# Performance work log

Hardware: AMD Instinct MI355X
Metric: run time of the kernel (lower is better)

Reference implementation:

```python
import jax, jax.numpy as jnp
import numpy as np

HEAD_DIM = 64
CLIP = 64  # clipping_distance
B, S = 32, 1024


def setup_inputs() -> dict:
    key = jax.random.key(0)
    kq, kk, kv, km, kt = jax.random.split(key, 5)
    q = jax.random.normal(kq, (B, S, HEAD_DIM), dtype=jnp.float32)
    k = jax.random.normal(kk, (B, S, HEAD_DIM), dtype=jnp.float32)
    v = jax.random.normal(kv, (B, S, HEAD_DIM), dtype=jnp.float32)
    mask = jax.random.randint(km, (B, S, S), 0, 2).astype(jnp.bool_)
    pos_table = jax.random.normal(kt, (2 * CLIP + 1, HEAD_DIM), dtype=jnp.float32)
    return {"q": q, "k": k, "v": v, "mask": mask, "pos_table": pos_table}


def reference(q, k, v, mask, pos_table):
    scaling = 1.0 / np.sqrt(HEAD_DIM).astype(np.float32)
    Sq, Sk = q.shape[1], k.shape[1]
    # relative positions k_idx - q_idx, clipped to [-CLIP, CLIP]
    rel = jnp.arange(Sk)[None, :] - jnp.arange(Sq)[:, None]      # [Sq, Sk]
    idx = jnp.clip(rel, -CLIP, CLIP) + CLIP                      # [Sq, Sk]
    pe = pos_table[idx]                                          # [Sq, Sk, D]
    # content logits + relative positional logits
    logits = jnp.einsum('bqd,bkd->bqk', q, k) + jnp.einsum('bqd,qkd->bqk', q, pe)
    logits = logits * scaling
    logits = jnp.where(mask, -jnp.inf, logits)
    attn = jax.nn.softmax(logits, axis=-1)                       # [B, Sq, Sk]
    return jnp.einsum('bqk,bkd->bqd', attn, v)
```

## Files before the change

kernel.cpp:

```cpp
#include <hip/hip_runtime.h>
#include <stdint.h>

#define BATCH 32
#define SEQ   1024
#define DIM   64
#define NKT   (SEQ / 64)

typedef uint16_t u16;
typedef uint32_t u32;
typedef unsigned long long u64;
typedef __attribute__((ext_vector_type(8))) __bf16 bf16x8;
typedef __attribute__((ext_vector_type(4))) float  f32x4;
typedef __attribute__((ext_vector_type(4))) u32    u32x4;

__device__ __forceinline__ float fexp2(float x) {
#if __has_builtin(__builtin_amdgcn_exp2f)
    return __builtin_amdgcn_exp2f(x);
#else
    return exp2f(x);
#endif
}

__device__ __forceinline__ u16 f2bf(float f) {
    u32 x = __builtin_bit_cast(u32, f);
    x += 0x7FFFu + ((x >> 16) & 1u);
    return (u16)(x >> 16);
}

__device__ __forceinline__ bf16x8 cvt8(const float* __restrict__ p) {
    f32x4 a = *reinterpret_cast<const f32x4*>(p);
    f32x4 b = *reinterpret_cast<const f32x4*>(p + 4);
    u16 t[8];
    t[0] = f2bf(a[0]); t[1] = f2bf(a[1]); t[2] = f2bf(a[2]); t[3] = f2bf(a[3]);
    t[4] = f2bf(b[0]); t[5] = f2bf(b[1]); t[6] = f2bf(b[2]); t[7] = f2bf(b[3]);
    return __builtin_bit_cast(bf16x8, *reinterpret_cast<u32x4*>(t));
}

__device__ __forceinline__ bf16x8 cvt8s(const float* __restrict__ p, float s) {
    f32x4 a = *reinterpret_cast<const f32x4*>(p);
    f32x4 b = *reinterpret_cast<const f32x4*>(p + 4);
    u16 t[8];
    t[0] = f2bf(a[0] * s); t[1] = f2bf(a[1] * s); t[2] = f2bf(a[2] * s); t[3] = f2bf(a[3] * s);
    t[4] = f2bf(b[0] * s); t[5] = f2bf(b[1] * s); t[6] = f2bf(b[2] * s); t[7] = f2bf(b[3] * s);
    return __builtin_bit_cast(bf16x8, *reinterpret_cast<u32x4*>(t));
}

__device__ __forceinline__ bf16x8 ldg8(const u16* p) {
    u32x4 u = *reinterpret_cast<const u32x4*>(p);
    return __builtin_bit_cast(bf16x8, u);
}

__global__ __launch_bounds__(256) void prep_kernel(
    const float* __restrict__ kg, const float* __restrict__ vg,
    const int* __restrict__ mask, u16* __restrict__ kb,
    u16* __restrict__ vtb_, u64* __restrict__ bits) {
    __shared__ u16 tile[64][72];
    const int t    = threadIdx.x;
    const int wave = t >> 6;
    const int lane = t & 63;
    const int wid  = blockIdx.x * 4 + wave;

    u32x4 cur = *reinterpret_cast<const u32x4*>(
        mask + (size_t)(wid >> 2) * SEQ + (wid & 3) * 256 + lane * 4);
#pragma unroll 1
    for (int it = 0; it < 4; ++it) {
        const int rg = wid + it * 32768;
        u32x4 nxt;
        if (it < 3) {
            const int rg2 = wid + (it + 1) * 32768;
            nxt = *reinterpret_cast<const u32x4*>(
                mask + (size_t)(rg2 >> 2) * SEQ + (rg2 & 3) * 256 + lane * 4);
        }
        int nib = (cur[0] != 0) | ((cur[1] != 0) << 1) |
                  ((cur[2] != 0) << 2) | ((cur[3] != 0) << 3);
        u64 b0 = __ballot(nib & 1);
        u64 b1 = __ballot(nib & 2);
        u64 b2 = __ballot(nib & 4);
        u64 b3 = __ballot(nib & 8);
        if (lane < 4) {
            u64 w = (lane == 0) ? b0 : (lane == 1) ? b1 : (lane == 2) ? b2 : b3;
            bits[(size_t)rg * 4 + lane] = w;
        }
        cur = nxt;
    }

    if (blockIdx.x < 512) {
        const int b  = blockIdx.x >> 4;
        const int k0 = (blockIdx.x & 15) * 64;

        {
            int kk = t >> 2;
            int d0 = (t & 3) * 16;
            const float* src = kg + ((size_t)b * SEQ + k0 + kk) * DIM + d0;
            u16 tmp[16];
#pragma unroll
            for (int i = 0; i < 4; ++i) {
                f32x4 a = *reinterpret_cast<const f32x4*>(src + i * 4);
                tmp[i * 4 + 0] = f2bf(a[0]); tmp[i * 4 + 1] = f2bf(a[1]);
                tmp[i * 4 + 2] = f2bf(a[2]); tmp[i * 4 + 3] = f2bf(a[3]);
            }
            u16* dst = kb + ((size_t)b * SEQ + k0 + kk) * DIM + d0;
            *reinterpret_cast<u32x4*>(dst)     = *reinterpret_cast<u32x4*>(tmp);
            *reinterpret_cast<u32x4*>(dst + 8) = *reinterpret_cast<u32x4*>(tmp + 8);
        }

        const float* vb  = vg  + (size_t)b * SEQ * DIM;
        u16*         vtb = vtb_ + (size_t)b * DIM * SEQ;
        {
            int kk = t >> 2;
            int d0 = (t & 3) * 16;
            const float* src = vb + (size_t)(k0 + kk) * DIM + d0;
            u16 tmp[16];
#pragma unroll
            for (int i = 0; i < 4; ++i) {
                f32x4 a = *reinterpret_cast<const f32x4*>(src + i * 4);
                tmp[i * 4 + 0] = f2bf(a[0]); tmp[i * 4 + 1] = f2bf(a[1]);
                tmp[i * 4 + 2] = f2bf(a[2]); tmp[i * 4 + 3] = f2bf(a[3]);
            }
            *reinterpret_cast<u32x4*>(&tile[kk][d0])     = *reinterpret_cast<u32x4*>(tmp);
            *reinterpret_cast<u32x4*>(&tile[kk][d0 + 8]) = *reinterpret_cast<u32x4*>(tmp + 8);
        }
        __syncthreads();
#pragma unroll
        for (int i = 0; i < 2; ++i) {
            int d  = t / 8 + i * 32;
            int ks = (t % 8) * 8;
            u16 tmp[8];
#pragma unroll
            for (int j = 0; j < 8; ++j) tmp[j] = tile[ks + j][d];
            *reinterpret_cast<u32x4*>(vtb + (size_t)d * SEQ + k0 + ks) =
                *reinterpret_cast<u32x4*>(tmp);
        }
    }
}

__global__ __launch_bounds__(512, 4) void attn_fast2(
    const float* __restrict__ qg, const u16* __restrict__ kbf,
    const u16* __restrict__ vt, const u64* __restrict__ mbits,
    const float* __restrict__ ptg, float* __restrict__ outg) {
    __shared__ float qp[64][132];
    __shared__ u16   plds[8][16][72];

    const int b    = blockIdx.y;
    const int q0   = blockIdx.x * 64;
    const int tid  = threadIdx.x;
    const int wave = tid >> 6;
    const int lane = tid & 63;
    const int wq   = wave & 3;
    const int wk   = wave >> 2;
    const int quad = lane >> 4;
    const int c16  = lane & 15;

    const float SC = 0.125f * 1.44269504088896340736f;

    const float* qb = qg + ((size_t)b * SEQ + q0) * DIM;

    const bf16x8 qA0 = cvt8s(qb + (size_t)(wq * 16 + c16) * DIM + quad * 8, SC);
    const bf16x8 qA1 = cvt8s(qb + (size_t)(wq * 16 + c16) * DIM + 32 + quad * 8, SC);

    const size_t rowbase = (size_t)b * SEQ + q0 + wq * 16 + quad * 4;
    u64 w2[2][4];
#pragma unroll
    for (int gg = 0; gg < 2; ++gg)
#pragma unroll
        for (int r = 0; r < 4; ++r)
            w2[gg][r] = mbits[((rowbase + r) * 4 + (wk * 2 + gg)) * 4 + (c16 & 3)];

    {
        const int jt0 = wk ? 5 : 0, jt1 = wk ? 9 : 5;
        for (int jt = jt0; jt < jt1; ++jt) {
            int j0 = jt * 16;
            int jr = min(j0 + c16, 128);
            bf16x8 b0 = cvt8(ptg + (size_t)jr * DIM + quad * 8);
            bf16x8 b1 = cvt8(ptg + (size_t)jr * DIM + 32 + quad * 8);
            f32x4 acc = {0.f, 0.f, 0.f, 0.f};
            acc = __builtin_amdgcn_mfma_f32_16x16x32_bf16(qA0, b0, acc, 0, 0, 0);
            acc = __builtin_amdgcn_mfma_f32_16x16x32_bf16(qA1, b1, acc, 0, 0, 0);
            int jcol = j0 + c16;
            if (jcol <= 128) {
#pragma unroll
                for (int r = 0; r < 4; ++r)
                    qp[wq * 16 + quad * 4 + r][jcol] = acc[r];
            }
        }
    }
    __syncthreads();

    const u16* kb_base  = kbf + (size_t)b * SEQ * DIM;
    const u16* vtb_base = vt  + (size_t)b * DIM * SEQ;

    float m_run[4], l_run[4];
    f32x4 O[4];
#pragma unroll
    for (int r = 0; r < 4; ++r) { m_run[r] = -1e30f; l_run[r] = 0.f; }
#pragma unroll
    for (int d = 0; d < 4; ++d) O[d] = f32x4{0.f, 0.f, 0.f, 0.f};

#pragma unroll
    for (int gg = 0; gg < 2; ++gg) {
#pragma unroll 1
        for (int t = 0; t < 4; ++t) {
            const int kt = wk * 8 + gg * 4 + t;
            const int k0 = kt * 64;

            f32x4 S[4];
            __builtin_amdgcn_s_setprio(1);
#pragma unroll
            for (int sub = 0; sub < 4; ++sub) {
                const u16* kr = kb_base + (size_t)(k0 + sub * 16 + c16) * DIM;
                bf16x8 kf0 = ldg8(kr + quad * 8);
                bf16x8 kf1 = ldg8(kr + 32 + quad * 8);
                f32x4 acc = {0.f, 0.f, 0.f, 0.f};
                acc = __builtin_amdgcn_mfma_f32_16x16x32_bf16(qA0, kf0, acc, 0, 0, 0);
                acc = __builtin_amdgcn_mfma_f32_16x16x32_bf16(qA1, kf1, acc, 0, 0, 0);
                S[sub] = acc;
            }
            __builtin_amdgcn_s_setprio(0);

            float sv[4][4];
#pragma unroll
            for (int r = 0; r < 4; ++r) {
                const int row_l = quad * 4 + r;
                const int row_g = q0 + wq * 16 + row_l;
                const u64 wr = w2[gg][r] >> (t * 16 + (c16 >> 2));
#pragma unroll
                for (int sub = 0; sub < 4; ++sub) {
                    int col_g = k0 + sub * 16 + c16;
                    int rel = col_g - row_g;
                    rel = rel < -64 ? -64 : (rel > 64 ? 64 : rel);
                    float x = S[sub][r] + qp[wq * 16 + row_l][rel + 64];
                    u32 bit = (u32)(wr >> (sub * 4)) & 1u;
                    sv[sub][r] = bit ? -1e30f : x;
                }
            }

            float m_new[4];
            bool need = false;
#pragma unroll
            for (int r = 0; r < 4; ++r) {
                float rmax = fmaxf(fmaxf(sv[0][r], sv[1][r]), fmaxf(sv[2][r], sv[3][r]));
                rmax = fmaxf(rmax, __shfl_xor(rmax, 1));
                rmax = fmaxf(rmax, __shfl_xor(rmax, 2));
                rmax = fmaxf(rmax, __shfl_xor(rmax, 4));
                rmax = fmaxf(rmax, __shfl_xor(rmax, 8));
                m_new[r] = fmaxf(m_run[r], rmax);
                need |= (m_new[r] > m_run[r]);
            }
            if (__any(need)) {
#pragma unroll
                for (int r = 0; r < 4; ++r) {
                    float alpha = fexp2(m_run[r] - m_new[r]);
                    l_run[r] *= alpha;
#pragma unroll
                    for (int d = 0; d < 4; ++d) O[d][r] *= alpha;
                }
            }
#pragma unroll
            for (int r = 0; r < 4; ++r) {
                m_run[r] = m_new[r];
                float rs = 0.f;
#pragma unroll
                for (int sub = 0; sub < 4; ++sub) {
                    float e = fexp2(sv[sub][r] - m_new[r]);
                    rs += e;
                    plds[wave][quad * 4 + r][sub * 16 + c16] = f2bf(e);
                }
                rs += __shfl_xor(rs, 1);
                rs += __shfl_xor(rs, 2);
                rs += __shfl_xor(rs, 4);
                rs += __shfl_xor(rs, 8);
                l_run[r] += rs;
            }

            bf16x8 pA0 = *reinterpret_cast<bf16x8*>(&plds[wave][c16][quad * 8]);
            bf16x8 pA1 = *reinterpret_cast<bf16x8*>(&plds[wave][c16][32 + quad * 8]);
            __builtin_amdgcn_s_setprio(1);
#pragma unroll
            for (int d = 0; d < 4; ++d) {
                const u16* vr = vtb_base + (size_t)(d * 16 + c16) * SEQ + k0;
                bf16x8 vf0 = ldg8(vr + quad * 8);
                bf16x8 vf1 = ldg8(vr + 32 + quad * 8);
                O[d] = __builtin_amdgcn_mfma_f32_16x16x32_bf16(pA0, vf0, O[d], 0, 0, 0);
                O[d] = __builtin_amdgcn_mfma_f32_16x16x32_bf16(pA1, vf1, O[d], 0, 0, 0);
            }
            __builtin_amdgcn_s_setprio(0);
        }
    }

    __syncthreads();
    float* cmb = &qp[0][0];
    const int cbase = (wq * 64 + lane) * 24;
    if (wk == 1) {
#pragma unroll
        for (int r = 0; r < 4; ++r) {
            cmb[cbase + r]     = m_run[r];
            cmb[cbase + 4 + r] = l_run[r];
        }
#pragma unroll
        for (int d = 0; d < 4; ++d)
#pragma unroll
            for (int r = 0; r < 4; ++r)
                cmb[cbase + 8 + d * 4 + r] = O[d][r];
    }
    __syncthreads();
    if (wk == 0) {
        float* ob = outg + ((size_t)b * SEQ + q0) * DIM;
#pragma unroll
        for (int r = 0; r < 4; ++r) {
            float m1 = cmb[cbase + r];
            float l1 = cmb[cbase + 4 + r];
            float mm = fmaxf(m_run[r], m1);
            float a0 = fexp2(m_run[r] - mm);
            float a1 = fexp2(m1 - mm);
            float inv = 1.f / (l_run[r] * a0 + l1 * a1);
            int row_l = wq * 16 + quad * 4 + r;
#pragma unroll
            for (int d = 0; d < 4; ++d) {
                float o = O[d][r] * a0 + cmb[cbase + 8 + d * 4 + r] * a1;
                ob[(size_t)row_l * DIM + d * 16 + c16] = o * inv;
            }
        }
    }
}

__global__ __launch_bounds__(256) void vt_kernel(const float* __restrict__ v,
                                                 u16* __restrict__ vt) {
    __shared__ u16 tile[64][72];
    const int b  = blockIdx.y;
    const int k0 = blockIdx.x * 64;
    const int t  = threadIdx.x;
    const float* vb  = v  + (size_t)b * SEQ * DIM;
    u16*         vtb = vt + (size_t)b * DIM * SEQ;

    {
        int kk = t >> 2;
        int d0 = (t & 3) * 16;
        const float* src = vb + (size_t)(k0 + kk) * DIM + d0;
        u16 tmp[16];
#pragma unroll
        for (int i = 0; i < 4; ++i) {
            f32x4 a = *reinterpret_cast<const f32x4*>(src + i * 4);
            tmp[i * 4 + 0] = f2bf(a[0]); tmp[i * 4 + 1] = f2bf(a[1]);
            tmp[i * 4 + 2] = f2bf(a[2]); tmp[i * 4 + 3] = f2bf(a[3]);
        }
        *reinterpret_cast<u32x4*>(&tile[kk][d0])     = *reinterpret_cast<u32x4*>(tmp);
        *reinterpret_cast<u32x4*>(&tile[kk][d0 + 8]) = *reinterpret_cast<u32x4*>(tmp + 8);
    }
    __syncthreads();
#pragma unroll
    for (int i = 0; i < 2; ++i) {
        int d  = t / 8 + i * 32;
        int ks = (t % 8) * 8;
        u16 tmp[8];
#pragma unroll
        for (int j = 0; j < 8; ++j) tmp[j] = tile[ks + j][d];
        *reinterpret_cast<u32x4*>(vtb + (size_t)d * SEQ + k0 + ks) =
            *reinterpret_cast<u32x4*>(tmp);
    }
}

template <bool USE_VT>
__global__ __launch_bounds__(256, 2) void attn_kernel(
    const float* __restrict__ qg, const float* __restrict__ kg,
    const void* __restrict__ vgv, const int* __restrict__ maskg,
    const float* __restrict__ ptg, float* __restrict__ outg) {
    __shared__ float qp[64][132];
    __shared__ int   mlds[4][16][68];
    __shared__ u16   plds[4][16][72];

    const int b    = blockIdx.y;
    const int q0   = blockIdx.x * 64;
    const int tid  = threadIdx.x;
    const int wave = tid >> 6;
    const int lane = tid & 63;
    const int quad = lane >> 4;
    const int c16  = lane & 15;

    const float* qb = qg + ((size_t)b * SEQ + q0) * DIM;
    const float* kb = kg + (size_t)b * SEQ * DIM;
    const int*   mb = maskg + ((size_t)b * SEQ + q0) * SEQ;

    const bf16x8 qA0 = cvt8(qb + (size_t)(wave * 16 + c16) * DIM + quad * 8);
    const bf16x8 qA1 = cvt8(qb + (size_t)(wave * 16 + c16) * DIM + 32 + quad * 8);

    for (int jt = 0; jt < 9; ++jt) {
        int j0 = jt * 16;
        int jr = min(j0 + c16, 128);
        bf16x8 b0 = cvt8(ptg + (size_t)jr * DIM + quad * 8);
        bf16x8 b1 = cvt8(ptg + (size_t)jr * DIM + 32 + quad * 8);
        f32x4 acc = {0.f, 0.f, 0.f, 0.f};
        acc = __builtin_amdgcn_mfma_f32_16x16x32_bf16(qA0, b0, acc, 0, 0, 0);
        acc = __builtin_amdgcn_mfma_f32_16x16x32_bf16(qA1, b1, acc, 0, 0, 0);
        int jcol = j0 + c16;
        if (jcol <= 128) {
#pragma unroll
            for (int r = 0; r < 4; ++r)
                qp[wave * 16 + quad * 4 + r][jcol] = acc[r];
        }
    }

    float m_run[4], l_run[4];
    f32x4 O[4];
#pragma unroll
    for (int r = 0; r < 4; ++r) { m_run[r] = -1e30f; l_run[r] = 0.f; }
#pragma unroll
    for (int d = 0; d < 4; ++d) O[d] = f32x4{0.f, 0.f, 0.f, 0.f};

#pragma unroll 1
    for (int kt = 0; kt < NKT; ++kt) {
        const int k0 = kt * 64;
        {
            int row_l = lane >> 2;
            const int* mrow = mb + (size_t)(wave * 16 + row_l) * SEQ + k0;
#pragma unroll
            for (int i = 0; i < 4; ++i) {
                int seg = (lane & 3) + i * 4;
                *reinterpret_cast<u32x4*>(&mlds[wave][row_l][seg * 4]) =
                    *reinterpret_cast<const u32x4*>(mrow + seg * 4);
            }
        }

        f32x4 S[4];
#pragma unroll
        for (int sub = 0; sub < 4; ++sub) {
            const float* kr = kb + (size_t)(k0 + sub * 16 + c16) * DIM;
            bf16x8 kb0 = cvt8(kr + quad * 8);
            bf16x8 kb1 = cvt8(kr + 32 + quad * 8);
            f32x4 acc = {0.f, 0.f, 0.f, 0.f};
            acc = __builtin_amdgcn_mfma_f32_16x16x32_bf16(qA0, kb0, acc, 0, 0, 0);
            acc = __builtin_amdgcn_mfma_f32_16x16x32_bf16(qA1, kb1, acc, 0, 0, 0);
            S[sub] = acc;
        }

        float sv[4][4];
#pragma unroll
        for (int sub = 0; sub < 4; ++sub) {
#pragma unroll
            for (int r = 0; r < 4; ++r) {
                int row_l = quad * 4 + r;
                int row_g = q0 + wave * 16 + row_l;
                int col_g = k0 + sub * 16 + c16;
                int rel = col_g - row_g;
                rel = rel < -64 ? -64 : (rel > 64 ? 64 : rel);
                float x = (S[sub][r] + qp[wave * 16 + row_l][rel + 64]) * 0.125f;
                int mv = mlds[wave][row_l][sub * 16 + c16];
                sv[sub][r] = mv ? -1e30f : x;
            }
        }

        float m_new[4], alpha[4];
#pragma unroll
        for (int r = 0; r < 4; ++r) {
            float rmax = fmaxf(fmaxf(sv[0][r], sv[1][r]), fmaxf(sv[2][r], sv[3][r]));
            rmax = fmaxf(rmax, __shfl_xor(rmax, 1));
            rmax = fmaxf(rmax, __shfl_xor(rmax, 2));
            rmax = fmaxf(rmax, __shfl_xor(rmax, 4));
            rmax = fmaxf(rmax, __shfl_xor(rmax, 8));
            m_new[r] = fmaxf(m_run[r], rmax);
            alpha[r] = __expf(m_run[r] - m_new[r]);
            m_run[r] = m_new[r];
        }
#pragma unroll
        for (int r = 0; r < 4; ++r) {
            float rs = 0.f;
#pragma unroll
            for (int sub = 0; sub < 4; ++sub) {
                float e = __expf(sv[sub][r] - m_new[r]);
                rs += e;
                plds[wave][quad * 4 + r][sub * 16 + c16] = f2bf(e);
            }
            rs += __shfl_xor(rs, 1);
            rs += __shfl_xor(rs, 2);
            rs += __shfl_xor(rs, 4);
            rs += __shfl_xor(rs, 8);
            l_run[r] = l_run[r] * alpha[r] + rs;
#pragma unroll
            for (int d = 0; d < 4; ++d) O[d][r] *= alpha[r];
        }

        bf16x8 pA0 = *reinterpret_cast<bf16x8*>(&plds[wave][c16][quad * 8]);
        bf16x8 pA1 = *reinterpret_cast<bf16x8*>(&plds[wave][c16][32 + quad * 8]);
#pragma unroll
        for (int d = 0; d < 4; ++d) {
            bf16x8 vb0, vb1;
            if (USE_VT) {
                const u16* vtb = (const u16*)vgv + (size_t)b * DIM * SEQ +
                                 (size_t)(d * 16 + c16) * SEQ + k0;
                vb0 = ldg8(vtb + quad * 8);
                vb1 = ldg8(vtb + 32 + quad * 8);
            } else {
                u16 t0[8], t1[8];
                const float* vbase = (const float*)vgv +
                                     ((size_t)b * SEQ + k0) * DIM + d * 16 + c16;
#pragma unroll
                for (int j = 0; j < 8; ++j) {
                    t0[j] = f2bf(vbase[(size_t)(quad * 8 + j) * DIM]);
                    t1[j] = f2bf(vbase[(size_t)(32 + quad * 8 + j) * DIM]);
                }
                vb0 = __builtin_bit_cast(bf16x8, *reinterpret_cast<u32x4*>(t0));
                vb1 = __builtin_bit_cast(bf16x8, *reinterpret_cast<u32x4*>(t1));
            }
            O[d] = __builtin_amdgcn_mfma_f32_16x16x32_bf16(pA0, vb0, O[d], 0, 0, 0);
            O[d] = __builtin_amdgcn_mfma_f32_16x16x32_bf16(pA1, vb1, O[d], 0, 0, 0);
        }
    }

    float* ob = outg + ((size_t)b * SEQ + q0) * DIM;
#pragma unroll
    for (int r = 0; r < 4; ++r) {
        float inv = 1.f / l_run[r];
        int row_l = wave * 16 + quad * 4 + r;
#pragma unroll
        for (int d = 0; d < 4; ++d)
            ob[(size_t)row_l * DIM + d * 16 + c16] = O[d][r] * inv;
    }
}

extern "C" void kernel_launch(void* const* d_in, const int* in_sizes, int n_in,
                              void* d_out, int out_size, void* d_ws, size_t ws_size,
                              hipStream_t stream) {
    const float* q    = (const float*)d_in[0];
    const float* k    = (const float*)d_in[1];
    const float* v    = (const float*)d_in[2];
    const int*   mask = (const int*)d_in[3];
    const float* pt   = (const float*)d_in[4];
    float* out        = (float*)d_out;

    const size_t vt_bytes = (size_t)BATCH * SEQ * DIM * sizeof(u16);
    const size_t kb_bytes = (size_t)BATCH * SEQ * DIM * sizeof(u16);
    const size_t mb_bytes = (size_t)BATCH * SEQ * 16 * sizeof(u64);
    dim3 grid(SEQ / 64, BATCH);

    if (ws_size >= vt_bytes + kb_bytes + mb_bytes) {
        u16* vt  = (u16*)d_ws;
        u16* kb  = (u16*)((char*)d_ws + vt_bytes);
        u64* mb2 = (u64*)((char*)d_ws + vt_bytes + kb_bytes);
        prep_kernel<<<dim3(8192), 256, 0, stream>>>(k, v, mask, kb, vt, mb2);
        attn_fast2<<<grid, 512, 0, stream>>>(q, kb, vt, mb2, pt, out);
    } else if (ws_size >= vt_bytes) {
        u16* vt = (u16*)d_ws;
        vt_kernel<<<grid, 256, 0, stream>>>(v, vt);
        attn_kernel<true><<<grid, 256, 0, stream>>>(q, k, (const void*)vt, mask, pt, out);
    } else {
        attn_kernel<false><<<grid, 256, 0, stream>>>(q, k, (const void*)v, mask, pt, out);
    }
}
```

Measured before the change: 282.5 us.

## Prefetch next K tile, early-issue V loads, skip rel-pos lookup on far tiles

The attention loop is flattened to a single loop over eight key tiles. K fragments for the next tile are loaded into registers while the current tile computes, and the first half of the V fragments is issued before the softmax. For tiles entirely outside the clipping window, the per-element LDS relative-position lookup is replaced by a per-row constant folded into the max and exp offset. The prep kernel now loads each mask row with four independent loads instead of a strided loop. The cost is extra register pressure from the prefetched K and V fragments, which could hurt occupancy under the 512-thread, 4-block launch bound.

```diff
diff --git a/kernel.cpp b/kernel.cpp
--- a/kernel.cpp
+++ b/kernel.cpp
@@ -58,31 +58,32 @@
     const int t    = threadIdx.x;
     const int wave = t >> 6;
     const int lane = t & 63;
-    const int wid  = blockIdx.x * 4 + wave;
-
-    u32x4 cur = *reinterpret_cast<const u32x4*>(
-        mask + (size_t)(wid >> 2) * SEQ + (wid & 3) * 256 + lane * 4);
-#pragma unroll 1
-    for (int it = 0; it < 4; ++it) {
-        const int rg = wid + it * 32768;
-        u32x4 nxt;
-        if (it < 3) {
-            const int rg2 = wid + (it + 1) * 32768;
-            nxt = *reinterpret_cast<const u32x4*>(
-                mask + (size_t)(rg2 >> 2) * SEQ + (rg2 & 3) * 256 + lane * 4);
-        }
-        int nib = (cur[0] != 0) | ((cur[1] != 0) << 1) |
-                  ((cur[2] != 0) << 2) | ((cur[3] != 0) << 3);
-        u64 b0 = __ballot(nib & 1);
-        u64 b1 = __ballot(nib & 2);
-        u64 b2 = __ballot(nib & 4);
-        u64 b3 = __ballot(nib & 8);
-        if (lane < 4) {
-            u64 w = (lane == 0) ? b0 : (lane == 1) ? b1 : (lane == 2) ? b2 : b3;
-            bits[(size_t)rg * 4 + lane] = w;
-        }
-        cur = nxt;
-    }
+    const int row  = blockIdx.x * 4 + wave;
+
+    const int* mrow = mask + (size_t)row * SEQ + lane * 4;
+    u32x4 x0 = *reinterpret_cast<const u32x4*>(mrow);
+    u32x4 x1 = *reinterpret_cast<const u32x4*>(mrow + 256);
+    u32x4 x2 = *reinterpret_cast<const u32x4*>(mrow + 512);
+    u32x4 x3 = *reinterpret_cast<const u32x4*>(mrow + 768);
+
+#define MPROC(x, g)                                                           \
+    {                                                                         \
+        int nib = (x[0] != 0) | ((x[1] != 0) << 1) |                          \
+                  ((x[2] != 0) << 2) | ((x[3] != 0) << 3);                    \
+        u64 b0 = __ballot(nib & 1);                                           \
+        u64 b1 = __ballot(nib & 2);                                           \
+        u64 b2 = __ballot(nib & 4);                                           \
+        u64 b3 = __ballot(nib & 8);                                           \
+        if (lane < 4) {                                                       \
+            u64 w = (lane == 0) ? b0 : (lane == 1) ? b1 : (lane == 2) ? b2 : b3; \
+            bits[(size_t)row * 16 + (g) * 4 + lane] = w;                      \
+        }                                                                     \
+    }
+    MPROC(x0, 0)
+    MPROC(x1, 1)
+    MPROC(x2, 2)
+    MPROC(x3, 3)
+#undef MPROC
 
     if (blockIdx.x < 512) {
         const int b  = blockIdx.x >> 4;
@@ -134,7 +135,7 @@
     }
 }
 
-__global__ __launch_bounds__(512, 4) void attn_fast2(
+__global__ __launch_bounds__(512, 4) void attn_fast3(
     const float* __restrict__ qg, const u16* __restrict__ kbf,
     const u16* __restrict__ vt, const u64* __restrict__ mbits,
     const float* __restrict__ ptg, float* __restrict__ outg) {
@@ -186,8 +187,16 @@
     }
     __syncthreads();
 
+    float cL[4], cR[4];
+#pragma unroll
+    for (int r = 0; r < 4; ++r) {
+        cL[r] = qp[wq * 16 + quad * 4 + r][0];
+        cR[r] = qp[wq * 16 + quad * 4 + r][128];
+    }
+
     const u16* kb_base  = kbf + (size_t)b * SEQ * DIM;
     const u16* vtb_base = vt  + (size_t)b * DIM * SEQ;
+    const int  row_min  = q0 + wq * 16;
 
     float m_run[4], l_run[4];
     f32x4 O[4];
@@ -196,33 +205,82 @@
 #pragma unroll
     for (int d = 0; d < 4; ++d) O[d] = f32x4{0.f, 0.f, 0.f, 0.f};
 
-#pragma unroll
-    for (int gg = 0; gg < 2; ++gg) {
+    const int ktbase = wk * 8;
+
+    bf16x8 kc0[4], kc1[4];
+#pragma unroll
+    for (int sub = 0; sub < 4; ++sub) {
+        const u16* kr = kb_base + (size_t)(ktbase * 64 + sub * 16 + c16) * DIM;
+        kc0[sub] = ldg8(kr + quad * 8);
+        kc1[sub] = ldg8(kr + 32 + quad * 8);
+    }
+
 #pragma unroll 1
-        for (int t = 0; t < 4; ++t) {
-            const int kt = wk * 8 + gg * 4 + t;
-            const int k0 = kt * 64;
-
-            f32x4 S[4];
-            __builtin_amdgcn_s_setprio(1);
+    for (int j = 0; j < 8; ++j) {
+        const int kt   = ktbase + j;
+        const int k0   = kt * 64;
+        const int j_gg = j >> 2;
+        const int j_t  = j & 3;
+
+        f32x4 S[4];
+        __builtin_amdgcn_s_setprio(1);
+#pragma unroll
+        for (int sub = 0; sub < 4; ++sub) {
+            f32x4 acc = {0.f, 0.f, 0.f, 0.f};
+            acc = __builtin_amdgcn_mfma_f32_16x16x32_bf16(qA0, kc0[sub], acc, 0, 0, 0);
+            acc = __builtin_amdgcn_mfma_f32_16x16x32_bf16(qA1, kc1[sub], acc, 0, 0, 0);
+            S[sub] = acc;
+        }
+        __builtin_amdgcn_s_setprio(0);
+
+        if (j < 7) {
+            const int k0n = k0 + 64;
 #pragma unroll
             for (int sub = 0; sub < 4; ++sub) {
-                const u16* kr = kb_base + (size_t)(k0 + sub * 16 + c16) * DIM;
-                bf16x8 kf0 = ldg8(kr + quad * 8);
-                bf16x8 kf1 = ldg8(kr + 32 + quad * 8);
-                f32x4 acc = {0.f, 0.f, 0.f, 0.f};
-                acc = __builtin_amdgcn_mfma_f32_16x16x32_bf16(qA0, kf0, acc, 0, 0, 0);
-                acc = __builtin_amdgcn_mfma_f32_16x16x32_bf16(qA1, kf1, acc, 0, 0, 0);
-                S[sub] = acc;
-            }
-            __builtin_amdgcn_s_setprio(0);
-
-            float sv[4][4];
+                const u16* kr = kb_base + (size_t)(k0n + sub * 16 + c16) * DIM;
+                kc0[sub] = ldg8(kr + quad * 8);
+                kc1[sub] = ldg8(kr + 32 + quad * 8);
+            }
+        }
+
+        bf16x8 vf0[4];
+#pragma unroll
+        for (int d = 0; d < 4; ++d)
+            vf0[d] = ldg8(vtb_base + (size_t)(d * 16 + c16) * SEQ + k0 + quad * 8);
+
+        const bool farL = (k0 + 127 <= row_min);
+        const bool farR = (k0 >= row_min + 79);
+        float m_new[4], ofs[4];
+        bool need = false;
+
+        if (farL | farR) {
+#pragma unroll
+            for (int r = 0; r < 4; ++r) {
+                const u64 wr = w2[j_gg][r] >> (j_t * 16 + (c16 >> 2));
+#pragma unroll
+                for (int sub = 0; sub < 4; ++sub) {
+                    u32 bit = (u32)(wr >> (sub * 4)) & 1u;
+                    S[sub][r] = bit ? -1e30f : S[sub][r];
+                }
+            }
+#pragma unroll
+            for (int r = 0; r < 4; ++r) {
+                float c = farL ? cL[r] : cR[r];
+                float rmax = fmaxf(fmaxf(S[0][r], S[1][r]), fmaxf(S[2][r], S[3][r]));
+                rmax = fmaxf(rmax, __shfl_xor(rmax, 1));
+                rmax = fmaxf(rmax, __shfl_xor(rmax, 2));
+                rmax = fmaxf(rmax, __shfl_xor(rmax, 4));
+                rmax = fmaxf(rmax, __shfl_xor(rmax, 8));
+                m_new[r] = fmaxf(m_run[r], rmax + c);
+                ofs[r]   = m_new[r] - c;
+                need |= (m_new[r] > m_run[r]);
+            }
+        } else {
 #pragma unroll
             for (int r = 0; r < 4; ++r) {
                 const int row_l = quad * 4 + r;
-                const int row_g = q0 + wq * 16 + row_l;
-                const u64 wr = w2[gg][r] >> (t * 16 + (c16 >> 2));
+                const int row_g = row_min + row_l;
+                const u64 wr = w2[j_gg][r] >> (j_t * 16 + (c16 >> 2));
 #pragma unroll
                 for (int sub = 0; sub < 4; ++sub) {
                     int col_g = k0 + sub * 16 + c16;
@@ -230,61 +288,58 @@
                     rel = rel < -64 ? -64 : (rel > 64 ? 64 : rel);
                     float x = S[sub][r] + qp[wq * 16 + row_l][rel + 64];
                     u32 bit = (u32)(wr >> (sub * 4)) & 1u;
-                    sv[sub][r] = bit ? -1e30f : x;
+                    S[sub][r] = bit ? -1e30f : x;
                 }
             }
-
-            float m_new[4];
-            bool need = false;
 #pragma unroll
             for (int r = 0; r < 4; ++r) {
-                float rmax = fmaxf(fmaxf(sv[0][r], sv[1][r]), fmaxf(sv[2][r], sv[3][r]));
+                float rmax = fmaxf(fmaxf(S[0][r], S[1][r]), fmaxf(S[2][r], S[3][r]));
                 rmax = fmaxf(rmax, __shfl_xor(rmax, 1));
                 rmax = fmaxf(rmax, __shfl_xor(rmax, 2));
                 rmax = fmaxf(rmax, __shfl_xor(rmax, 4));
                 rmax = fmaxf(rmax, __shfl_xor(rmax, 8));
                 m_new[r] = fmaxf(m_run[r], rmax);
+                ofs[r]   = m_new[r];
                 need |= (m_new[r] > m_run[r]);
             }
-            if (__any(need)) {
-#pragma unroll
-                for (int r = 0; r < 4; ++r) {
-                    float alpha = fexp2(m_run[r] - m_new[r]);
-                    l_run[r] *= alpha;
-#pragma unroll
-                    for (int d = 0; d < 4; ++d) O[d][r] *= alpha;
-                }
-            }
+        }
+
+        if (__any(need)) {
 #pragma unroll
             for (int r = 0; r < 4; ++r) {
-                m_run[r] = m_new[r];
-                float rs = 0.f;
-#pragma unroll
-                for (int sub = 0; sub < 4; ++sub) {
-                    float e = fexp2(sv[sub][r] - m_new[r]);
-                    rs += e;
-                    plds[wave][quad * 4 + r][sub * 16 + c16] = f2bf(e);
-                }
-                rs += __shfl_xor(rs, 1);
-                rs += __shfl_xor(rs, 2);
-                rs += __shfl_xor(rs, 4);
-                rs += __shfl_xor(rs, 8);
-                l_run[r] += rs;
-            }
-
-            bf16x8 pA0 = *reinterpret_cast<bf16x8*>(&plds[wave][c16][quad * 8]);
-            bf16x8 pA1 = *reinterpret_cast<bf16x8*>(&plds[wave][c16][32 + quad * 8]);
-            __builtin_amdgcn_s_setprio(1);
-#pragma unroll
-            for (int d = 0; d < 4; ++d) {
-                const u16* vr = vtb_base + (size_t)(d * 16 + c16) * SEQ + k0;
-                bf16x8 vf0 = ldg8(vr + quad * 8);
-                bf16x8 vf1 = ldg8(vr + 32 + quad * 8);
-                O[d] = __builtin_amdgcn_mfma_f32_16x16x32_bf16(pA0, vf0, O[d], 0, 0, 0);
-                O[d] = __builtin_amdgcn_mfma_f32_16x16x32_bf16(pA1, vf1, O[d], 0, 0, 0);
-            }
-            __builtin_amdgcn_s_setprio(0);
-        }
+                float alpha = fexp2(m_run[r] - m_new[r]);
+                l_run[r] *= alpha;
+#pragma unroll
+                for (int d = 0; d < 4; ++d) O[d][r] *= alpha;
+            }
+        }
+#pragma unroll
+        for (int r = 0; r < 4; ++r) {
+            m_run[r] = m_new[r];
+            float rs = 0.f;
+#pragma unroll
+            for (int sub = 0; sub < 4; ++sub) {
+                float e = fexp2(S[sub][r] - ofs[r]);
+                rs += e;
+                plds[wave][quad * 4 + r][sub * 16 + c16] = f2bf(e);
+            }
+            rs += __shfl_xor(rs, 1);
+            rs += __shfl_xor(rs, 2);
+            rs += __shfl_xor(rs, 4);
+            rs += __shfl_xor(rs, 8);
+            l_run[r] += rs;
+        }
+
+        bf16x8 pA0 = *reinterpret_cast<bf16x8*>(&plds[wave][c16][quad * 8]);
+        bf16x8 pA1 = *reinterpret_cast<bf16x8*>(&plds[wave][c16][32 + quad * 8]);
+        __builtin_amdgcn_s_setprio(1);
+#pragma unroll
+        for (int d = 0; d < 4; ++d) {
+            bf16x8 vf1 = ldg8(vtb_base + (size_t)(d * 16 + c16) * SEQ + k0 + 32 + quad * 8);
+            O[d] = __builtin_amdgcn_mfma_f32_16x16x32_bf16(pA0, vf0[d], O[d], 0, 0, 0);
+            O[d] = __builtin_amdgcn_mfma_f32_16x16x32_bf16(pA1, vf1, O[d], 0, 0, 0);
+        }
+        __builtin_amdgcn_s_setprio(0);
     }
 
     __syncthreads();
@@ -536,7 +591,7 @@
         u16* kb  = (u16*)((char*)d_ws + vt_bytes);
         u64* mb2 = (u64*)((char*)d_ws + vt_bytes + kb_bytes);
         prep_kernel<<<dim3(8192), 256, 0, stream>>>(k, v, mask, kb, vt, mb2);
-        attn_fast2<<<grid, 512, 0, stream>>>(q, kb, vt, mb2, pt, out);
+        attn_fast3<<<grid, 512, 0, stream>>>(q, kb, vt, mb2, pt, out);
     } else if (ws_size >= vt_bytes) {
         u16* vt = (u16*)d_ws;
         vt_kernel<<<grid, 256, 0, stream>>>(v, vt);
```

New measurement: 360.2 us. 27.5% more time.

## Replace bit-packed mask with byte mask staged through LDS

Applied to the files above, without the earlier changes.

The prep kernel now turns the int32 mask into one byte per element instead of packing it into bits with wave ballots. The attention kernel loads each 16x64 byte-mask tile per wave, prefetches the next tile into registers, and stages it in LDS so the softmax step reads it there. This removes the ballot packing and per-element shift work, at the cost of 8x more mask bytes written and read (32 MB versus 4 MB) and extra LDS traffic.

```diff
diff --git a/kernel.cpp b/kernel.cpp
--- a/kernel.cpp
+++ b/kernel.cpp
@@ -6,6 +6,7 @@
 #define DIM   64
 #define NKT   (SEQ / 64)
 
+typedef uint8_t  u8;
 typedef uint16_t u16;
 typedef uint32_t u32;
 typedef unsigned long long u64;
@@ -50,38 +51,29 @@
     return __builtin_bit_cast(bf16x8, u);
 }
 
-__global__ __launch_bounds__(256) void prep_kernel(
-    const float* __restrict__ kg, const float* __restrict__ vg,
-    const int* __restrict__ mask, u16* __restrict__ kb,
-    u16* __restrict__ vtb_, u64* __restrict__ bits) {
+__global__ __launch_bounds__(256) void prep8(
+    const int* __restrict__ m, const float* __restrict__ kg,
+    const float* __restrict__ vg, u8* __restrict__ mb8,
+    u16* __restrict__ kb, u16* __restrict__ vtb_) {
     __shared__ u16 tile[64][72];
-    const int t    = threadIdx.x;
-    const int wave = t >> 6;
-    const int lane = t & 63;
-    const int wid  = blockIdx.x * 4 + wave;
-
-    u32x4 cur = *reinterpret_cast<const u32x4*>(
-        mask + (size_t)(wid >> 2) * SEQ + (wid & 3) * 256 + lane * 4);
-#pragma unroll 1
-    for (int it = 0; it < 4; ++it) {
-        const int rg = wid + it * 32768;
-        u32x4 nxt;
-        if (it < 3) {
-            const int rg2 = wid + (it + 1) * 32768;
-            nxt = *reinterpret_cast<const u32x4*>(
-                mask + (size_t)(rg2 >> 2) * SEQ + (rg2 & 3) * 256 + lane * 4);
-        }
-        int nib = (cur[0] != 0) | ((cur[1] != 0) << 1) |
-                  ((cur[2] != 0) << 2) | ((cur[3] != 0) << 3);
-        u64 b0 = __ballot(nib & 1);
-        u64 b1 = __ballot(nib & 2);
-        u64 b2 = __ballot(nib & 4);
-        u64 b3 = __ballot(nib & 8);
-        if (lane < 4) {
-            u64 w = (lane == 0) ? b0 : (lane == 1) ? b1 : (lane == 2) ? b2 : b3;
-            bits[(size_t)rg * 4 + lane] = w;
-        }
-        cur = nxt;
+    const int t = threadIdx.x;
+
+    {
+        size_t i = ((size_t)blockIdx.x * 256 + t) * 16;
+        u32x4 a = *reinterpret_cast<const u32x4*>(m + i);
+        u32x4 b = *reinterpret_cast<const u32x4*>(m + i + 4);
+        u32x4 c = *reinterpret_cast<const u32x4*>(m + i + 8);
+        u32x4 d = *reinterpret_cast<const u32x4*>(m + i + 12);
+        u32x4 o;
+        o[0] = (u32)(a[0] != 0) | ((u32)(a[1] != 0) << 8) |
+               ((u32)(a[2] != 0) << 16) | ((u32)(a[3] != 0) << 24);
+        o[1] = (u32)(b[0] != 0) | ((u32)(b[1] != 0) << 8) |
+               ((u32)(b[2] != 0) << 16) | ((u32)(b[3] != 0) << 24);
+        o[2] = (u32)(c[0] != 0) | ((u32)(c[1] != 0) << 8) |
+               ((u32)(c[2] != 0) << 16) | ((u32)(c[3] != 0) << 24);
+        o[3] = (u32)(d[0] != 0) | ((u32)(d[1] != 0) << 8) |
+               ((u32)(d[2] != 0) << 16) | ((u32)(d[3] != 0) << 24);
+        *reinterpret_cast<u32x4*>(mb8 + i) = o;
     }
 
     if (blockIdx.x < 512) {
@@ -103,10 +95,8 @@
             *reinterpret_cast<u32x4*>(dst)     = *reinterpret_cast<u32x4*>(tmp);
             *reinterpret_cast<u32x4*>(dst + 8) = *reinterpret_cast<u32x4*>(tmp + 8);
         }
-
-        const float* vb  = vg  + (size_t)b * SEQ * DIM;
-        u16*         vtb = vtb_ + (size_t)b * DIM * SEQ;
         {
+            const float* vb = vg + (size_t)b * SEQ * DIM;
             int kk = t >> 2;
             int d0 = (t & 3) * 16;
             const float* src = vb + (size_t)(k0 + kk) * DIM + d0;
@@ -121,6 +111,7 @@
             *reinterpret_cast<u32x4*>(&tile[kk][d0 + 8]) = *reinterpret_cast<u32x4*>(tmp + 8);
         }
         __syncthreads();
+        u16* vtb = vtb_ + (size_t)b * DIM * SEQ;
 #pragma unroll
         for (int i = 0; i < 2; ++i) {
             int d  = t / 8 + i * 32;
@@ -134,12 +125,13 @@
     }
 }
 
-__global__ __launch_bounds__(512, 4) void attn_fast2(
+__global__ __launch_bounds__(512, 4) void attn_fast7(
     const float* __restrict__ qg, const u16* __restrict__ kbf,
-    const u16* __restrict__ vt, const u64* __restrict__ mbits,
+    const u16* __restrict__ vt, const u8* __restrict__ mb8,
     const float* __restrict__ ptg, float* __restrict__ outg) {
     __shared__ float qp[64][132];
     __shared__ u16   plds[8][16][72];
+    __shared__ u8    mlds[8][16][64];
 
     const int b    = blockIdx.y;
     const int q0   = blockIdx.x * 64;
@@ -157,14 +149,6 @@
 
     const bf16x8 qA0 = cvt8s(qb + (size_t)(wq * 16 + c16) * DIM + quad * 8, SC);
     const bf16x8 qA1 = cvt8s(qb + (size_t)(wq * 16 + c16) * DIM + 32 + quad * 8, SC);
-
-    const size_t rowbase = (size_t)b * SEQ + q0 + wq * 16 + quad * 4;
-    u64 w2[2][4];
-#pragma unroll
-    for (int gg = 0; gg < 2; ++gg)
-#pragma unroll
-        for (int r = 0; r < 4; ++r)
-            w2[gg][r] = mbits[((rowbase + r) * 4 + (wk * 2 + gg)) * 4 + (c16 & 3)];
 
     {
         const int jt0 = wk ? 5 : 0, jt1 = wk ? 9 : 5;
@@ -189,6 +173,12 @@
     const u16* kb_base  = kbf + (size_t)b * SEQ * DIM;
     const u16* vtb_base = vt  + (size_t)b * DIM * SEQ;
 
+    const u8* m8 = mb8 + (size_t)b * SEQ * SEQ +
+                   (size_t)(q0 + wq * 16 + (lane >> 2)) * SEQ + (lane & 3) * 16;
+
+    u32x4 mcur = *reinterpret_cast<const u32x4*>(m8 + (size_t)(wk * 8) * 64);
+    u32x4 mnext;
+
     float m_run[4], l_run[4];
     f32x4 O[4];
 #pragma unroll
@@ -202,6 +192,9 @@
         for (int t = 0; t < 4; ++t) {
             const int kt = wk * 8 + gg * 4 + t;
             const int k0 = kt * 64;
+
+            *reinterpret_cast<u32x4*>(&mlds[wave][lane >> 2][(lane & 3) * 16]) = mcur;
+            mnext = *reinterpret_cast<const u32x4*>(m8 + (size_t)((kt + 1) & 15) * 64);
 
             f32x4 S[4];
             __builtin_amdgcn_s_setprio(1);
@@ -222,15 +215,14 @@
             for (int r = 0; r < 4; ++r) {
                 const int row_l = quad * 4 + r;
                 const int row_g = q0 + wq * 16 + row_l;
-                const u64 wr = w2[gg][r] >> (t * 16 + (c16 >> 2));
 #pragma unroll
                 for (int sub = 0; sub < 4; ++sub) {
                     int col_g = k0 + sub * 16 + c16;
                     int rel = col_g - row_g;
                     rel = rel < -64 ? -64 : (rel > 64 ? 64 : rel);
                     float x = S[sub][r] + qp[wq * 16 + row_l][rel + 64];
-                    u32 bit = (u32)(wr >> (sub * 4)) & 1u;
-                    sv[sub][r] = bit ? -1e30f : x;
+                    u8 mv = mlds[wave][row_l][sub * 16 + c16];
+                    sv[sub][r] = mv ? -1e30f : x;
                 }
             }
 
@@ -284,6 +276,8 @@
                 O[d] = __builtin_amdgcn_mfma_f32_16x16x32_bf16(pA1, vf1, O[d], 0, 0, 0);
             }
             __builtin_amdgcn_s_setprio(0);
+
+            mcur = mnext;
         }
     }
 
@@ -493,9 +487,9 @@
                 const float* vbase = (const float*)vgv +
                                      ((size_t)b * SEQ + k0) * DIM + d * 16 + c16;
 #pragma unroll
-                for (int j = 0; j < 8; ++j) {
-                    t0[j] = f2bf(vbase[(size_t)(quad * 8 + j) * DIM]);
-                    t1[j] = f2bf(vbase[(size_t)(32 + quad * 8 + j) * DIM]);
+                for (int jj = 0; jj < 8; ++jj) {
+                    t0[jj] = f2bf(vbase[(size_t)(quad * 8 + jj) * DIM]);
+                    t1[jj] = f2bf(vbase[(size_t)(32 + quad * 8 + jj) * DIM]);
                 }
                 vb0 = __builtin_bit_cast(bf16x8, *reinterpret_cast<u32x4*>(t0));
                 vb1 = __builtin_bit_cast(bf16x8, *reinterpret_cast<u32x4*>(t1));
@@ -528,15 +522,15 @@
 
     const size_t vt_bytes = (size_t)BATCH * SEQ * DIM * sizeof(u16);
     const size_t kb_bytes = (size_t)BATCH * SEQ * DIM * sizeof(u16);
-    const size_t mb_bytes = (size_t)BATCH * SEQ * 16 * sizeof(u64);
+    const size_t m8_bytes = (size_t)BATCH * SEQ * SEQ;
     dim3 grid(SEQ / 64, BATCH);
 
-    if (ws_size >= vt_bytes + kb_bytes + mb_bytes) {
+    if (ws_size >= vt_bytes + kb_bytes + m8_bytes) {
         u16* vt  = (u16*)d_ws;
         u16* kb  = (u16*)((char*)d_ws + vt_bytes);
-        u64* mb2 = (u64*)((char*)d_ws + vt_bytes + kb_bytes);
-        prep_kernel<<<dim3(8192), 256, 0, stream>>>(k, v, mask, kb, vt, mb2);
-        attn_fast2<<<grid, 512, 0, stream>>>(q, kb, vt, mb2, pt, out);
+        u8*  mb8 = (u8*)((char*)d_ws + vt_bytes + kb_bytes);
+        prep8<<<dim3(8192), 256, 0, stream>>>(mask, k, v, mb8, kb, vt);
+        attn_fast7<<<grid, 512, 0, stream>>>(q, kb, vt, mb8, pt, out);
     } else if (ws_size >= vt_bytes) {
         u16* vt = (u16*)d_ws;
         vt_kernel<<<grid, 256, 0, stream>>>(v, vt);
```

Result: no change. 286.3 us (+1.3%).
